# Optimization experiments

Measured on AMD Instinct MI355X. Metric: run time of the kernel, lower is better.

The kernel has to match this reference:

```python
import math
import jax, jax.numpy as jnp
import numpy as np

EMBED_SIZE = 1024
NUM_HEADS = 16
HEAD_DIM = EMBED_SIZE // NUM_HEADS
N, L = 8, 1024
MASK_FILL = -1e3  # value used by masked_fill in the original (NOT -inf)
SCALE = 1.0 / math.sqrt(EMBED_SIZE)  # original divides by embed_size**0.5, not head_dim


def setup_inputs() -> dict:
    key = jax.random.key(0)
    ks = jax.random.split(key, 7)
    values = jax.random.normal(ks[0], (N, L, EMBED_SIZE), dtype=jnp.float32)
    keys_t = jax.random.normal(ks[1], (N, L, EMBED_SIZE), dtype=jnp.float32)
    queries = jax.random.normal(ks[2], (N, L, EMBED_SIZE), dtype=jnp.float32)
    attn_mask = jax.random.randint(ks[3], (1, 1, L, L), 0, 2, dtype=jnp.int32)
    scr_key_padding_mask = jax.random.randint(ks[4], (N, 1, 1, L), 0, 2, dtype=jnp.int32)
    # fc_out: nn.Linear(embed_size, embed_size) with bias
    fc_w = jax.random.normal(ks[5], (EMBED_SIZE, EMBED_SIZE), dtype=jnp.float32) * (1.0 / math.sqrt(EMBED_SIZE))
    fc_b = jax.random.normal(ks[6], (EMBED_SIZE,), dtype=jnp.float32) * 0.01
    return {"values": values, "keys": keys_t, "queries": queries,
            "fc_w": fc_w, "fc_b": fc_b,
            "attn_mask": attn_mask, "scr_key_padding_mask": scr_key_padding_mask}


def reference(values, keys, queries, fc_w, fc_b, attn_mask, scr_key_padding_mask):
    n, q_len, e = queries.shape
    k_len = keys.shape[1]
    h, d = NUM_HEADS, HEAD_DIM
    # NOTE: the original defines per-head Linear projections but never applies them
    v = values.reshape(n, k_len, h, d)
    k = keys.reshape(n, k_len, h, d)
    q = queries.reshape(n, q_len, h, d)
    energy = jnp.einsum('nqhd,nkhd->nhqk', q, k)  # [n, h, q, k]
    am = attn_mask[:, :, :k_len, :k_len]
    energy = jnp.where(am == 0, MASK_FILL, energy)
    energy = jnp.where(scr_key_padding_mask == 0, MASK_FILL, energy)
    attention = jax.nn.softmax(energy * SCALE, axis=3)
    out = jnp.einsum('nhql,nlhd->nqhd', attention, v).reshape(n, q_len, h * d)
    return out @ fc_w.T + fc_b
```

## Files before the change

kernel.cpp:

```cpp
#include <hip/hip_runtime.h>

#define L_SEQ 1024
#define EMB 1024
#define NH 16
#define HD 64

typedef _Float16 half8 __attribute__((ext_vector_type(8)));
typedef _Float16 half4v __attribute__((ext_vector_type(4)));
typedef float f32x4 __attribute__((ext_vector_type(4)));
typedef float fvec4 __attribute__((ext_vector_type(4)));
typedef unsigned int u32;
typedef unsigned long long u64;

constexpr float C2 = 0.045084220027780106f;

constexpr int PP = 72;

__device__ __forceinline__ void async16(const void* g, void* l) {
    __builtin_amdgcn_global_load_lds((const __attribute__((address_space(1))) u32*)g,
                                     (__attribute__((address_space(3))) u32*)l, 16, 0, 0);
}

__global__ void pack_mask_kernel(const int* __restrict__ am, u32* __restrict__ bits) {
    const int i = blockIdx.x * 256 + threadIdx.x;
    const int lane = threadIdx.x & 63;
    u64 b = __ballot(am[i] != 0);
    if (lane == 0)       bits[i >> 5] = (u32)b;
    else if (lane == 32) bits[i >> 5] = (u32)(b >> 32);
}

__global__ void combine_mask_kernel(const u32* __restrict__ abits,
                                    const u32* __restrict__ pbits,
                                    u32* __restrict__ cmb) {
    const int tid = threadIdx.x;
    const int w = tid & 31, qq = tid >> 5;
    const int q = blockIdx.x * 8 + qq;
    const u32 a = abits[q * 32 + w];
#pragma unroll
    for (int n = 0; n < 8; ++n)
        cmb[((size_t)(n * L_SEQ) + q) * 32 + w] = a & pbits[n * 32 + w];
}

__global__ void convert_w_kernel(const float* __restrict__ w, _Float16* __restrict__ o) {
    size_t i = ((size_t)blockIdx.x * blockDim.x + threadIdx.x) * 4;
    fvec4 v = *(const fvec4*)(w + i);
    half4v h;
#pragma unroll
    for (int j = 0; j < 4; ++j) h[j] = (_Float16)v[j];
    *(half4v*)(o + i) = h;
}

__global__ __launch_bounds__(256) void cvt_kv_kernel(
    const float* __restrict__ keys, const float* __restrict__ values,
    const int* __restrict__ pad_mask,
    _Float16* __restrict__ K16, _Float16* __restrict__ Vt16, u32* __restrict__ pbits)
{
    __shared__ __align__(16) _Float16 Vt[64 * PP];
    const int tid = threadIdx.x;
    const int kt = blockIdx.x, h = blockIdx.y, n = blockIdx.z;
    const int kbase = kt * 64;
    const int r = tid >> 2, c0 = (tid & 3) * 16;
    const int nh = n * NH + h;

    {
        const float* src = keys + ((size_t)(n * L_SEQ + kbase + r)) * EMB + h * HD + c0;
        fvec4 a0 = *(const fvec4*)(src),     a1 = *(const fvec4*)(src + 4);
        fvec4 a2 = *(const fvec4*)(src + 8), a3 = *(const fvec4*)(src + 12);
        half8 o0, o1;
#pragma unroll
        for (int j = 0; j < 4; ++j) {
            o0[j] = (_Float16)a0[j]; o0[j + 4] = (_Float16)a1[j];
            o1[j] = (_Float16)a2[j]; o1[j + 4] = (_Float16)a3[j];
        }
        _Float16* dst = K16 + ((size_t)nh * L_SEQ + kbase + r) * HD + c0;
        *(half8*)dst = o0; *(half8*)(dst + 8) = o1;
    }
    {
        const float* src = values + ((size_t)(n * L_SEQ + kbase + r)) * EMB + h * HD + c0;
        fvec4 vv[4];
        vv[0] = *(const fvec4*)(src);     vv[1] = *(const fvec4*)(src + 4);
        vv[2] = *(const fvec4*)(src + 8); vv[3] = *(const fvec4*)(src + 12);
#pragma unroll
        for (int i = 0; i < 16; ++i)
            Vt[(c0 + i) * PP + r] = (_Float16)vv[i >> 2][i & 3];
    }
    if (blockIdx.y == 0 && tid < 64) {
        u64 b = __ballot(pad_mask[(size_t)n * L_SEQ + kbase + tid] != 0);
        if (tid == 0)       pbits[n * 32 + kt * 2]     = (u32)b;
        else if (tid == 32) pbits[n * 32 + kt * 2 + 1] = (u32)(b >> 32);
    }
    __syncthreads();
    {
        const int d = tid >> 2, k0 = (tid & 3) * 16;
        half8 v0 = *(const half8*)(&Vt[d * PP + k0]);
        half8 v1 = *(const half8*)(&Vt[d * PP + k0 + 8]);
        _Float16* dst = Vt16 + ((size_t)nh * HD + d) * L_SEQ + kbase + k0;
        *(half8*)dst = v0; *(half8*)(dst + 8) = v1;
    }
}

__global__ __launch_bounds__(256, 4) void attn_kernel(
    const _Float16* __restrict__ K16, const _Float16* __restrict__ Vt16,
    const float* __restrict__ queries, const u32* __restrict__ cmb,
    _Float16* __restrict__ out_f16)
{
    __shared__ __align__(16) _Float16 K_lds[2][64 * 64];
    __shared__ __align__(16) _Float16 V_lds[2][64 * 64];

    const int tid = threadIdx.x;
    const int lane = tid & 63;
    const int wave = tid >> 6;
    const int l16 = lane & 15;
    const int quad = lane >> 4;
    const int bid = blockIdx.x;
    const int nh = bid & 127, qt = bid >> 7;
    const int n = nh >> 4, h = nh & 15;
    const int qbase = qt * 128;
    const int xr = l16 & 7;

    half8 qf[2][2];
#pragma unroll
    for (int s = 0; s < 2; ++s) {
        const int qrow = qbase + wave * 32 + s * 16 + l16;
        const float* qp = queries + ((size_t)(n * L_SEQ + qrow)) * EMB + h * HD;
#pragma unroll
        for (int t = 0; t < 2; ++t) {
            fvec4 a = *(const fvec4*)(qp + t * 32 + quad * 8);
            fvec4 b = *(const fvec4*)(qp + t * 32 + quad * 8 + 4);
#pragma unroll
            for (int j = 0; j < 4; ++j) {
                qf[s][t][j]     = (_Float16)(a[j] * C2);
                qf[s][t][j + 4] = (_Float16)(b[j] * C2);
            }
        }
    }

    f32x4 Ot[2][4];
#pragma unroll
    for (int s = 0; s < 2; ++s)
#pragma unroll
        for (int dt = 0; dt < 4; ++dt) Ot[s][dt] = (f32x4){0.f, 0.f, 0.f, 0.f};
    float lsum[2] = {0.f, 0.f};

    const _Float16* Kt_base = K16 + (size_t)nh * L_SEQ * HD;
    const _Float16* Vt_base = Vt16 + (size_t)nh * HD * L_SEQ;
    const int gch = (lane & 7) ^ ((lane >> 3) & 7);
    const int drow = (lane >> 3);
    const u32* mrow0 = cmb + ((size_t)(n * L_SEQ) + qbase + wave * 32 + l16) * 32;
    const u32* mrow1 = mrow0 + 16 * 32;

    const int voff_base = l16 * 64 + (quad & 1) * 4;

#pragma unroll
    for (int s2 = 0; s2 < 2; ++s2) {
        const int row = wave * 16 + s2 * 8 + drow;
        async16(Kt_base + (size_t)row * HD + gch * 8, &K_lds[0][(wave * 16 + s2 * 8) * 64]);
        async16(Vt_base + (size_t)row * L_SEQ + gch * 8, &V_lds[0][(wave * 16 + s2 * 8) * 64]);
    }

    for (int kt = 0; kt < L_SEQ / 64; ++kt) {
        const int cb = kt & 1;
        __syncthreads();

        if (kt < 15) {
            const int kb2 = (kt + 1) * 64;
#pragma unroll
            for (int s2 = 0; s2 < 2; ++s2) {
                const int row = wave * 16 + s2 * 8 + drow;
                async16(Kt_base + (size_t)(kb2 + row) * HD + gch * 8,
                        &K_lds[cb ^ 1][(wave * 16 + s2 * 8) * 64]);
                async16(Vt_base + (size_t)row * L_SEQ + kb2 + gch * 8,
                        &V_lds[cb ^ 1][(wave * 16 + s2 * 8) * 64]);
            }
        }
        const u32 w0a = mrow0[kt * 2], w1a = mrow0[kt * 2 + 1];
        const u32 w0b = mrow1[kt * 2], w1b = mrow1[kt * 2 + 1];

        f32x4 S[2][4];
#pragma unroll
        for (int s = 0; s < 2; ++s)
#pragma unroll
            for (int tj = 0; tj < 4; ++tj) S[s][tj] = (f32x4){0.f, 0.f, 0.f, 0.f};
#pragma unroll
        for (int tj = 0; tj < 4; ++tj) {
            const _Float16* kr = &K_lds[cb][(tj * 16 + l16) * 64];
            const int c0 = (quad ^ xr) * 8;
            half8 k0 = *(const half8*)(kr + c0);
            half8 k1 = *(const half8*)(kr + (c0 ^ 32));
            S[0][tj] = __builtin_amdgcn_mfma_f32_16x16x32_f16(k0, qf[0][0], S[0][tj], 0, 0, 0);
            S[0][tj] = __builtin_amdgcn_mfma_f32_16x16x32_f16(k1, qf[0][1], S[0][tj], 0, 0, 0);
            S[1][tj] = __builtin_amdgcn_mfma_f32_16x16x32_f16(k0, qf[1][0], S[1][tj], 0, 0, 0);
            S[1][tj] = __builtin_amdgcn_mfma_f32_16x16x32_f16(k1, qf[1][1], S[1][tj], 0, 0, 0);
        }

#pragma unroll
        for (int tj = 0; tj < 4; ++tj) {
            const int c = tj * 2 + (quad >> 1);
            half4v vf[4];
#pragma unroll
            for (int dt = 0; dt < 4; ++dt)
                vf[dt] = *(const half4v*)(&V_lds[cb][dt * 16 * 64 + voff_base + ((c ^ xr) * 8)]);

            half4v hp[2];
#pragma unroll
            for (int s = 0; s < 2; ++s) {
                const u32 pw0 = s ? w0b : w0a, pw1 = s ? w1b : w1a;
                const u32 m4 = ((tj & 2) ? pw1 : pw0) >> ((tj & 1) * 16 + quad * 4);
                float p[4];
#pragma unroll
                for (int reg = 0; reg < 4; ++reg) {
                    float z = __builtin_amdgcn_exp2f(S[s][tj][reg]);
                    int zi = __float_as_int(z) & (-(int)((m4 >> reg) & 1u));
                    p[reg] = __int_as_float(zi);
                }
                lsum[s] += (p[0] + p[1]) + (p[2] + p[3]);
                hp[s] = half4v{(_Float16)p[0], (_Float16)p[1], (_Float16)p[2], (_Float16)p[3]};
            }
#pragma unroll
            for (int dt = 0; dt < 4; ++dt) {
                Ot[0][dt] = __builtin_amdgcn_mfma_f32_16x16x16f16(vf[dt], hp[0], Ot[0][dt], 0, 0, 0);
                Ot[1][dt] = __builtin_amdgcn_mfma_f32_16x16x16f16(vf[dt], hp[1], Ot[1][dt], 0, 0, 0);
            }
        }
    }

#pragma unroll
    for (int s = 0; s < 2; ++s) {
        lsum[s] += __shfl_xor(lsum[s], 16);
        lsum[s] += __shfl_xor(lsum[s], 32);
    }
#pragma unroll
    for (int s = 0; s < 2; ++s) {
        const float linv = 1.0f / lsum[s];
        const int q = qbase + wave * 32 + s * 16 + l16;
        _Float16* op = out_f16 + ((size_t)(n * L_SEQ + q)) * EMB + h * HD;
#pragma unroll
        for (int dt = 0; dt < 4; ++dt) {
            half4v o;
#pragma unroll
            for (int reg = 0; reg < 4; ++reg) o[reg] = (_Float16)(Ot[s][dt][reg] * linv);
            *(half4v*)(op + dt * 16 + quad * 4) = o;
        }
    }
}

__global__ __launch_bounds__(256, 3) void fc_kernel(
    const _Float16* __restrict__ A, const _Float16* __restrict__ W,
    const float* __restrict__ bias, float* __restrict__ C)
{
    __shared__ __align__(16) _Float16 As[128 * 64];
    __shared__ __align__(16) _Float16 Ws[128 * 64];

    const int tid = threadIdx.x;
    const int lane = tid & 63;
    const int wv = tid >> 6;
    const int l16 = lane & 15;
    const int quad = lane >> 4;
    const int wm = (wv >> 1) * 64, wn = (wv & 1) * 64;
    const int Mb = blockIdx.x * 128, Nb = blockIdx.y * 128;
    const int gch = (lane & 7) ^ ((lane >> 3) & 7);
    const int drow = lane >> 3;
    const int xr = l16 & 7;

    f32x4 acc[4][4];
#pragma unroll
    for (int i = 0; i < 4; ++i)
#pragma unroll
        for (int j = 0; j < 4; ++j) acc[i][j] = (f32x4){0.f, 0.f, 0.f, 0.f};

    for (int k0 = 0; k0 < EMB; k0 += 64) {
        __syncthreads();
#pragma unroll
        for (int s = 0; s < 4; ++s) {
            const int row = wv * 32 + s * 8 + drow;
            async16(A + (size_t)(Mb + row) * EMB + k0 + gch * 8, &As[(wv * 32 + s * 8) * 64]);
            async16(W + (size_t)(Nb + row) * EMB + k0 + gch * 8, &Ws[(wv * 32 + s * 8) * 64]);
        }
        __syncthreads();

#pragma unroll
        for (int t = 0; t < 2; ++t) {
            half8 af[4], bf[4];
            const int c0 = ((t * 4 + quad) ^ xr) * 8;
#pragma unroll
            for (int i = 0; i < 4; ++i) {
                af[i] = *(const half8*)(&As[(wm + i * 16 + l16) * 64 + c0]);
                bf[i] = *(const half8*)(&Ws[(wn + i * 16 + l16) * 64 + c0]);
            }
#pragma unroll
            for (int i = 0; i < 4; ++i)
#pragma unroll
                for (int j = 0; j < 4; ++j)
                    acc[i][j] = __builtin_amdgcn_mfma_f32_16x16x32_f16(af[i], bf[j], acc[i][j], 0, 0, 0);
        }
    }

#pragma unroll
    for (int i = 0; i < 4; ++i) {
        const int m = Mb + wm + i * 16 + quad * 4;
#pragma unroll
        for (int j = 0; j < 4; ++j) {
            const int jc = Nb + wn + j * 16 + l16;
            const float b = bias[jc];
#pragma unroll
            for (int reg = 0; reg < 4; ++reg)
                C[(size_t)(m + reg) * EMB + jc] = acc[i][j][reg] + b;
        }
    }
}

extern "C" void kernel_launch(void* const* d_in, const int* in_sizes, int n_in,
                              void* d_out, int out_size, void* d_ws, size_t ws_size,
                              hipStream_t stream) {
    const float* values  = (const float*)d_in[0];
    const float* keys    = (const float*)d_in[1];
    const float* queries = (const float*)d_in[2];
    const float* fc_w    = (const float*)d_in[3];
    const float* fc_b    = (const float*)d_in[4];
    const int*   amask   = (const int*)d_in[5];
    const int*   pmask   = (const int*)d_in[6];
    float* out = (float*)d_out;

    char* w = (char*)d_ws;
    _Float16* attn_out = (_Float16*)w;
    _Float16* w_f16    = (_Float16*)(w + (size_t)16 * 1024 * 1024);
    u32*      abits    = (u32*)(w + (size_t)18 * 1024 * 1024);
    u32*      pbits    = (u32*)(w + (size_t)18 * 1024 * 1024 + 512 * 1024);
    u32*      cmb      = (u32*)(w + (size_t)19 * 1024 * 1024);
    _Float16* K16      = (_Float16*)(w + (size_t)20 * 1024 * 1024);
    _Float16* Vt16     = (_Float16*)(w + (size_t)36 * 1024 * 1024);

    pack_mask_kernel<<<4096, 256, 0, stream>>>(amask, abits);
    convert_w_kernel<<<1024, 256, 0, stream>>>(fc_w, w_f16);
    cvt_kv_kernel<<<dim3(16, 16, 8), 256, 0, stream>>>(keys, values, pmask, K16, Vt16, pbits);
    combine_mask_kernel<<<128, 256, 0, stream>>>(abits, pbits, cmb);
    attn_kernel<<<1024, 256, 0, stream>>>(K16, Vt16, queries, cmb, attn_out);
    fc_kernel<<<dim3(64, 8), 256, 0, stream>>>(attn_out, w_f16, fc_b, out);
}
```

Measured before the change: 269.9 us.

## Double-buffer fc GEMM tiles and interleave attention QK with softmax per tile

The fc GEMM now double-buffers its A and W tiles in LDS. It prefetches the next k-tile asynchronously while computing on the current one, which drops one barrier per iteration, and lowers the launch-bounds occupancy hint from 3 to 2 blocks. In the attention kernel, each 16-key sub-tile's score MFMAs now feed straight into exp, masking and the PV MFMAs, instead of computing all scores first. This lowers live score registers and gives more room to interleave. The cost is doubled LDS use in fc, which lowers occupancy, and the scheduler having less independent MFMA work per phase.

```diff
diff --git a/kernel.cpp b/kernel.cpp
--- a/kernel.cpp
+++ b/kernel.cpp
@@ -176,50 +176,45 @@
         const u32 w0a = mrow0[kt * 2], w1a = mrow0[kt * 2 + 1];
         const u32 w0b = mrow1[kt * 2], w1b = mrow1[kt * 2 + 1];
 
-        f32x4 S[2][4];
-#pragma unroll
-        for (int s = 0; s < 2; ++s)
-#pragma unroll
-            for (int tj = 0; tj < 4; ++tj) S[s][tj] = (f32x4){0.f, 0.f, 0.f, 0.f};
 #pragma unroll
         for (int tj = 0; tj < 4; ++tj) {
             const _Float16* kr = &K_lds[cb][(tj * 16 + l16) * 64];
             const int c0 = (quad ^ xr) * 8;
             half8 k0 = *(const half8*)(kr + c0);
             half8 k1 = *(const half8*)(kr + (c0 ^ 32));
-            S[0][tj] = __builtin_amdgcn_mfma_f32_16x16x32_f16(k0, qf[0][0], S[0][tj], 0, 0, 0);
-            S[0][tj] = __builtin_amdgcn_mfma_f32_16x16x32_f16(k1, qf[0][1], S[0][tj], 0, 0, 0);
-            S[1][tj] = __builtin_amdgcn_mfma_f32_16x16x32_f16(k0, qf[1][0], S[1][tj], 0, 0, 0);
-            S[1][tj] = __builtin_amdgcn_mfma_f32_16x16x32_f16(k1, qf[1][1], S[1][tj], 0, 0, 0);
-        }
-
-#pragma unroll
-        for (int tj = 0; tj < 4; ++tj) {
+
+            f32x4 S0 = (f32x4){0.f, 0.f, 0.f, 0.f};
+            f32x4 S1 = (f32x4){0.f, 0.f, 0.f, 0.f};
+            S0 = __builtin_amdgcn_mfma_f32_16x16x32_f16(k0, qf[0][0], S0, 0, 0, 0);
+            S0 = __builtin_amdgcn_mfma_f32_16x16x32_f16(k1, qf[0][1], S0, 0, 0, 0);
+            S1 = __builtin_amdgcn_mfma_f32_16x16x32_f16(k0, qf[1][0], S1, 0, 0, 0);
+            S1 = __builtin_amdgcn_mfma_f32_16x16x32_f16(k1, qf[1][1], S1, 0, 0, 0);
+
             const int c = tj * 2 + (quad >> 1);
             half4v vf[4];
 #pragma unroll
             for (int dt = 0; dt < 4; ++dt)
                 vf[dt] = *(const half4v*)(&V_lds[cb][dt * 16 * 64 + voff_base + ((c ^ xr) * 8)]);
 
-            half4v hp[2];
-#pragma unroll
-            for (int s = 0; s < 2; ++s) {
-                const u32 pw0 = s ? w0b : w0a, pw1 = s ? w1b : w1a;
-                const u32 m4 = ((tj & 2) ? pw1 : pw0) >> ((tj & 1) * 16 + quad * 4);
-                float p[4];
-#pragma unroll
-                for (int reg = 0; reg < 4; ++reg) {
-                    float z = __builtin_amdgcn_exp2f(S[s][tj][reg]);
-                    int zi = __float_as_int(z) & (-(int)((m4 >> reg) & 1u));
-                    p[reg] = __int_as_float(zi);
-                }
-                lsum[s] += (p[0] + p[1]) + (p[2] + p[3]);
-                hp[s] = half4v{(_Float16)p[0], (_Float16)p[1], (_Float16)p[2], (_Float16)p[3]};
-            }
+            const u32 m4a = (((tj & 2) ? w1a : w0a) >> ((tj & 1) * 16 + quad * 4));
+            const u32 m4b = (((tj & 2) ? w1b : w0b) >> ((tj & 1) * 16 + quad * 4));
+            float p0[4], p1[4];
+#pragma unroll
+            for (int reg = 0; reg < 4; ++reg) {
+                float za = __builtin_amdgcn_exp2f(S0[reg]);
+                float zb = __builtin_amdgcn_exp2f(S1[reg]);
+                p0[reg] = __int_as_float(__float_as_int(za) & (-(int)((m4a >> reg) & 1u)));
+                p1[reg] = __int_as_float(__float_as_int(zb) & (-(int)((m4b >> reg) & 1u)));
+            }
+            lsum[0] += (p0[0] + p0[1]) + (p0[2] + p0[3]);
+            lsum[1] += (p1[0] + p1[1]) + (p1[2] + p1[3]);
+            half4v hp0 = {(_Float16)p0[0], (_Float16)p0[1], (_Float16)p0[2], (_Float16)p0[3]};
+            half4v hp1 = {(_Float16)p1[0], (_Float16)p1[1], (_Float16)p1[2], (_Float16)p1[3]};
+
 #pragma unroll
             for (int dt = 0; dt < 4; ++dt) {
-                Ot[0][dt] = __builtin_amdgcn_mfma_f32_16x16x16f16(vf[dt], hp[0], Ot[0][dt], 0, 0, 0);
-                Ot[1][dt] = __builtin_amdgcn_mfma_f32_16x16x16f16(vf[dt], hp[1], Ot[1][dt], 0, 0, 0);
+                Ot[0][dt] = __builtin_amdgcn_mfma_f32_16x16x16f16(vf[dt], hp0, Ot[0][dt], 0, 0, 0);
+                Ot[1][dt] = __builtin_amdgcn_mfma_f32_16x16x16f16(vf[dt], hp1, Ot[1][dt], 0, 0, 0);
             }
         }
     }
@@ -244,12 +239,12 @@
     }
 }
 
-__global__ __launch_bounds__(256, 3) void fc_kernel(
+__global__ __launch_bounds__(256, 2) void fc_kernel(
     const _Float16* __restrict__ A, const _Float16* __restrict__ W,
     const float* __restrict__ bias, float* __restrict__ C)
 {
-    __shared__ __align__(16) _Float16 As[128 * 64];
-    __shared__ __align__(16) _Float16 Ws[128 * 64];
+    __shared__ __align__(16) _Float16 As[2][128 * 64];
+    __shared__ __align__(16) _Float16 Ws[2][128 * 64];
 
     const int tid = threadIdx.x;
     const int lane = tid & 63;
@@ -268,15 +263,28 @@
 #pragma unroll
         for (int j = 0; j < 4; ++j) acc[i][j] = (f32x4){0.f, 0.f, 0.f, 0.f};
 
-    for (int k0 = 0; k0 < EMB; k0 += 64) {
+#pragma unroll
+    for (int s = 0; s < 4; ++s) {
+        const int row = wv * 32 + s * 8 + drow;
+        async16(A + (size_t)(Mb + row) * EMB + gch * 8, &As[0][(wv * 32 + s * 8) * 64]);
+        async16(W + (size_t)(Nb + row) * EMB + gch * 8, &Ws[0][(wv * 32 + s * 8) * 64]);
+    }
+
+    for (int kt = 0; kt < EMB / 64; ++kt) {
+        const int cb = kt & 1;
         __syncthreads();
-#pragma unroll
-        for (int s = 0; s < 4; ++s) {
-            const int row = wv * 32 + s * 8 + drow;
-            async16(A + (size_t)(Mb + row) * EMB + k0 + gch * 8, &As[(wv * 32 + s * 8) * 64]);
-            async16(W + (size_t)(Nb + row) * EMB + k0 + gch * 8, &Ws[(wv * 32 + s * 8) * 64]);
-        }
-        __syncthreads();
+
+        if (kt < EMB / 64 - 1) {
+            const int k2 = (kt + 1) * 64;
+#pragma unroll
+            for (int s = 0; s < 4; ++s) {
+                const int row = wv * 32 + s * 8 + drow;
+                async16(A + (size_t)(Mb + row) * EMB + k2 + gch * 8,
+                        &As[cb ^ 1][(wv * 32 + s * 8) * 64]);
+                async16(W + (size_t)(Nb + row) * EMB + k2 + gch * 8,
+                        &Ws[cb ^ 1][(wv * 32 + s * 8) * 64]);
+            }
+        }
 
 #pragma unroll
         for (int t = 0; t < 2; ++t) {
@@ -284,8 +292,8 @@
             const int c0 = ((t * 4 + quad) ^ xr) * 8;
 #pragma unroll
             for (int i = 0; i < 4; ++i) {
-                af[i] = *(const half8*)(&As[(wm + i * 16 + l16) * 64 + c0]);
-                bf[i] = *(const half8*)(&Ws[(wn + i * 16 + l16) * 64 + c0]);
+                af[i] = *(const half8*)(&As[cb][(wm + i * 16 + l16) * 64 + c0]);
+                bf[i] = *(const half8*)(&Ws[cb][(wn + i * 16 + l16) * 64 + c0]);
             }
 #pragma unroll
             for (int i = 0; i < 4; ++i)
```

New measurement: 271.2 us. No clear change (+0.5%).
